# Kernel optimization log

Hardware: AMD Instinct MI355X
Metric: run time of the kernel (lower is better)

## Reference

```python
import jax, jax.numpy as jnp
import numpy as np

FEATS = 10
B, S, R = 64, 300, 100


def _linear_params(key, out_dim, in_dim):
    kw, kb = jax.random.split(key)
    bound = 1.0 / np.sqrt(in_dim)
    w = jax.random.uniform(kw, (out_dim, in_dim), jnp.float32, -bound, bound)
    b = jax.random.uniform(kb, (out_dim,), jnp.float32, -bound, bound)
    return w, b


def setup_inputs() -> dict:
    key = jax.random.key(0)
    ks = jax.random.split(key, 7)
    x = jax.random.normal(ks[0], (B, S, R, FEATS), jnp.float32)
    l1_w, l1_b = _linear_params(ks[1], 5, FEATS + 5)
    l2_w, l2_b = _linear_params(ks[2], 5, 5)
    l3_w, l3_b = _linear_params(ks[3], 5, 5)
    fc1_w, fc1_b = _linear_params(ks[4], 5, FEATS + 10)
    fc2_w, fc2_b = _linear_params(ks[5], 5, 5)
    fc3_w, fc3_b = _linear_params(ks[6], 1, 5)
    return {"x": x,
            "l1_w": l1_w, "l1_b": l1_b, "l2_w": l2_w, "l2_b": l2_b,
            "l3_w": l3_w, "l3_b": l3_b,
            "fc1_w": fc1_w, "fc1_b": fc1_b, "fc2_w": fc2_w, "fc2_b": fc2_b,
            "fc3_w": fc3_w, "fc3_b": fc3_b}


def reference(x, l1_w, l1_b, l2_w, l2_b, l3_w, l3_b,
              fc1_w, fc1_b, fc2_w, fc2_b, fc3_w, fc3_b):
    elu = jax.nn.elu
    bsz, seq, reads, _ = x.shape
    # dot of each read's first 4 feats with read 0's -> [B,S,R]
    r = jnp.sum(x[..., 0:4] * x[:, :, 0:1, 0:4], axis=-1)
    z = jnp.concatenate([r[..., None], x], axis=3)  # [B,S,R,feats+1]
    b = jnp.mean(x[..., 0:4], axis=2)               # [B,S,4]
    bexp = jnp.broadcast_to(b[:, :, None, :], (bsz, seq, reads, 4))
    bx = jnp.concatenate([bexp, z], axis=3)         # [B,S,R,feats+5]
    y = elu(jnp.einsum('bsrf,of->bsro', bx, l1_w) + l1_b)
    y = elu(jnp.einsum('bsrf,of->bsro', y, l2_w) + l2_b + y)
    y = elu(jnp.einsum('bsrf,of->bsro', y, l3_w) + l3_b + y)
    ymean = jnp.mean(y, axis=2, keepdims=True)      # [B,S,1,5]
    ymexp = jnp.broadcast_to(ymean, (bsz, seq, reads, 5))
    z2 = jnp.concatenate([ymexp, bx], axis=3)       # [B,S,R,feats+10]
    h = elu(jnp.einsum('bsrf,of->bsro', z2, fc1_w) + fc1_b)
    h = elu(jnp.einsum('bsrf,of->bsro', h, fc2_w) + fc2_b + h)
    h = 5.0 * elu(jnp.einsum('bsrf,of->bsro', h, fc3_w) + fc3_b)  # [B,S,R,1]
    out = jax.nn.sigmoid(jnp.max(h, axis=1))        # [B,R,1]
    return jnp.squeeze(out, axis=-1)                # [B,R]
```

## Files before the change

### kernel.cpp

```cpp
#include <hip/hip_runtime.h>
#include <math.h>

#define B 64
#define S 300
#define R 100
#define F 10
#define RF (R * F)
#define NTILE (B * S)
#define NWAVE (NTILE / 2)
#define NBLK (NWAVE / 4)

typedef float v2 __attribute__((ext_vector_type(2)));
typedef float v4 __attribute__((ext_vector_type(4)));

__device__ __forceinline__ v4 splat4(float s) { v4 r; r.x = s; r.y = s; r.z = s; r.w = s; return r; }
__device__ __forceinline__ v4 hsplat(float a, float b) { v4 r; r.x = a; r.y = a; r.z = b; r.w = b; return r; }
__device__ __forceinline__ v4 fma4(v4 a, float b, v4 c) {
    return __builtin_elementwise_fma(a, splat4(b), c);
}
__device__ __forceinline__ v4 fma4v(v4 a, v4 b, v4 c) {
    return __builtin_elementwise_fma(a, b, c);
}
__device__ __forceinline__ v4 elu4(v4 x) {
    v4 xm = __builtin_elementwise_min(x, splat4(0.f));
    v4 e;
    e.x = __expf(xm.x); e.y = __expf(xm.y); e.z = __expf(xm.z); e.w = __expf(xm.w);
    return __builtin_elementwise_max(x, e - splat4(1.f));
}

template <int CTRL>
__device__ __forceinline__ float dppadd(float v) {
    int t = __builtin_amdgcn_update_dpp(0, __float_as_int(v), CTRL, 0xF, 0xF, true);
    return v + __int_as_float(t);
}
__device__ __forceinline__ float wsum_dpp(float v) {
    v = dppadd<0x111>(v);
    v = dppadd<0x112>(v);
    v = dppadd<0x114>(v);
    v = dppadd<0x118>(v);
    v = dppadd<0x142>(v);
    v = dppadd<0x143>(v);
    return __uint_as_float(__builtin_amdgcn_readlane(__float_as_uint(v), 63));
}
__device__ __forceinline__ float rdlane0(float v) {
    return __uint_as_float(__builtin_amdgcn_readlane(__float_as_uint(v), 0));
}
__device__ __forceinline__ unsigned int fkey(float f) {
    unsigned int bits = __float_as_uint(f);
    return (bits & 0x80000000u) ? ~bits : (bits | 0x80000000u);
}

__global__ __launch_bounds__(256) void alt_pred_k1(
    const float* __restrict__ x,
    const float* __restrict__ l1_w, const float* __restrict__ l1_b,
    const float* __restrict__ l2_w, const float* __restrict__ l2_b,
    const float* __restrict__ l3_w, const float* __restrict__ l3_b,
    const float* __restrict__ fc1_w, const float* __restrict__ fc1_b,
    const float* __restrict__ fc2_w, const float* __restrict__ fc2_b,
    const float* __restrict__ fc3_w, const float* __restrict__ fc3_b,
    unsigned int* __restrict__ wsmax)
{
    const int tid = threadIdx.x;
    const int wv = tid >> 6;
    const int lane = tid & 63;
    const int gw = blockIdx.x * 4 + wv;
    const int t0 = gw * 2;
    const int b = t0 / S;
    const float* xA = x + (size_t)t0 * RF;
    const float* xB = xA + RF;

    const bool a2 = (lane < R - 64);
    const int r2 = a2 ? (lane + 64) : (R - 1);

    v4 f[F];
    {
        const float2* pA1 = (const float2*)(xA + lane * F);
        const float2* pA2 = (const float2*)(xA + r2 * F);
        const float2* pB1 = (const float2*)(xB + lane * F);
        const float2* pB2 = (const float2*)(xB + r2 * F);
#pragma unroll
        for (int i = 0; i < F; i += 2) {
            float2 a1 = pA1[i >> 1], a2v = pA2[i >> 1];
            float2 b1 = pB1[i >> 1], b2v = pB2[i >> 1];
            f[i].x = a1.x;     f[i].y = a2v.x; f[i].z = b1.x;     f[i].w = b2v.x;
            f[i + 1].x = a1.y; f[i + 1].y = a2v.y; f[i + 1].z = b1.y; f[i + 1].w = b2v.y;
        }
    }

    float x0A[4], x0B[4];
#pragma unroll
    for (int k = 0; k < 4; ++k) {
        x0A[k] = rdlane0(f[k].x);
        x0B[k] = rdlane0(f[k].z);
    }
    v4 rdot = f[3] * hsplat(x0A[3], x0B[3]);
    rdot = fma4v(f[2], hsplat(x0A[2], x0B[2]), rdot);
    rdot = fma4v(f[1], hsplat(x0A[1], x0B[1]), rdot);
    rdot = fma4v(f[0], hsplat(x0A[0], x0B[0]), rdot);

    float bmA[4], bmB[4];
#pragma unroll
    for (int k = 0; k < 4; ++k) {
        float locA = f[k].x + (a2 ? f[k].y : 0.f);
        float locB = f[k].z + (a2 ? f[k].w : 0.f);
        bmA[k] = wsum_dpp(locA) * (1.f / R);
        bmB[k] = wsum_dpp(locB) * (1.f / R);
    }

    v4 y1[5];
#pragma unroll
    for (int o = 0; o < 5; ++o) {
        float pA = l1_b[o], pB = l1_b[o];
#pragma unroll
        for (int k = 0; k < 4; ++k) {
            pA = fmaf(bmA[k], l1_w[o * 15 + k], pA);
            pB = fmaf(bmB[k], l1_w[o * 15 + k], pB);
        }
        v4 acc = hsplat(pA, pB);
        acc = fma4(rdot, l1_w[o * 15 + 4], acc);
#pragma unroll
        for (int k = 0; k < F; ++k) acc = fma4(f[k], l1_w[o * 15 + 5 + k], acc);
        y1[o] = elu4(acc);
    }
    v4 y2[5];
#pragma unroll
    for (int o = 0; o < 5; ++o) {
        v4 acc = splat4(l2_b[o]) + y1[o];
#pragma unroll
        for (int k = 0; k < 5; ++k) acc = fma4(y1[k], l2_w[o * 5 + k], acc);
        y2[o] = elu4(acc);
    }
    v4 y3[5];
#pragma unroll
    for (int o = 0; o < 5; ++o) {
        v4 acc = splat4(l3_b[o]) + y2[o];
#pragma unroll
        for (int k = 0; k < 5; ++k) acc = fma4(y2[k], l3_w[o * 5 + k], acc);
        y3[o] = elu4(acc);
    }

    float ymA[5], ymB[5];
#pragma unroll
    for (int k = 0; k < 5; ++k) {
        float locA = y3[k].x + (a2 ? y3[k].y : 0.f);
        float locB = y3[k].z + (a2 ? y3[k].w : 0.f);
        ymA[k] = wsum_dpp(locA) * (1.f / R);
        ymB[k] = wsum_dpp(locB) * (1.f / R);
    }

    v4 h1[5];
#pragma unroll
    for (int o = 0; o < 5; ++o) {
        float pA = fc1_b[o], pB = fc1_b[o];
#pragma unroll
        for (int k = 0; k < 5; ++k) {
            pA = fmaf(ymA[k], fc1_w[o * 20 + k], pA);
            pB = fmaf(ymB[k], fc1_w[o * 20 + k], pB);
        }
#pragma unroll
        for (int k = 0; k < 4; ++k) {
            pA = fmaf(bmA[k], fc1_w[o * 20 + 5 + k], pA);
            pB = fmaf(bmB[k], fc1_w[o * 20 + 5 + k], pB);
        }
        v4 acc = hsplat(pA, pB);
        acc = fma4(rdot, fc1_w[o * 20 + 9], acc);
#pragma unroll
        for (int k = 0; k < F; ++k) acc = fma4(f[k], fc1_w[o * 20 + 10 + k], acc);
        h1[o] = elu4(acc);
    }
    v4 h2[5];
#pragma unroll
    for (int o = 0; o < 5; ++o) {
        v4 acc = splat4(fc2_b[o]) + h1[o];
#pragma unroll
        for (int k = 0; k < 5; ++k) acc = fma4(h1[k], fc2_w[o * 5 + k], acc);
        h2[o] = elu4(acc);
    }
    v4 hacc = splat4(fc3_b[0]);
#pragma unroll
    for (int k = 0; k < 5; ++k) hacc = fma4(h2[k], fc3_w[k], hacc);

    const float m1 = fmaxf(hacc.x, hacc.z);
    const float m2 = fmaxf(hacc.y, hacc.w);
    atomicMax(&wsmax[b * R + lane], fkey(m1));
    if (a2) atomicMax(&wsmax[b * R + lane + 64], fkey(m2));
}

__global__ void alt_pred_k2(const unsigned int* __restrict__ wsmax,
                            float* __restrict__ out)
{
    const int i = blockIdx.x * blockDim.x + threadIdx.x;
    if (i < B * R) {
        const unsigned int key = wsmax[i];
        const unsigned int bits = (key & 0x80000000u) ? (key & 0x7FFFFFFFu) : ~key;
        const float acc = __uint_as_float(bits);
        const float h = 5.f * (acc > 0.f ? acc : (__expf(acc) - 1.f));
        out[i] = 1.f / (1.f + __expf(-h));
    }
}

extern "C" void kernel_launch(void* const* d_in, const int* in_sizes, int n_in,
                              void* d_out, int out_size, void* d_ws, size_t ws_size,
                              hipStream_t stream) {
    const float* x     = (const float*)d_in[0];
    const float* l1_w  = (const float*)d_in[1];
    const float* l1_b  = (const float*)d_in[2];
    const float* l2_w  = (const float*)d_in[3];
    const float* l2_b  = (const float*)d_in[4];
    const float* l3_w  = (const float*)d_in[5];
    const float* l3_b  = (const float*)d_in[6];
    const float* fc1_w = (const float*)d_in[7];
    const float* fc1_b = (const float*)d_in[8];
    const float* fc2_w = (const float*)d_in[9];
    const float* fc2_b = (const float*)d_in[10];
    const float* fc3_w = (const float*)d_in[11];
    const float* fc3_b = (const float*)d_in[12];

    unsigned int* wsmax = (unsigned int*)d_ws;
    hipMemsetAsync(d_ws, 0, (size_t)B * R * sizeof(unsigned int), stream);

    alt_pred_k1<<<NBLK, 256, 0, stream>>>(
        x, l1_w, l1_b, l2_w, l2_b, l3_w, l3_b,
        fc1_w, fc1_b, fc2_w, fc2_b, fc3_w, fc3_b, wsmax);

    alt_pred_k2<<<(B * R + 255) / 256, 256, 0, stream>>>(wsmax, (float*)d_out);
}
```

Measured before the change: 41.37 us.

## Repack per-lane data as float2 pairs, shrink blocks, load read0 directly

Reorganizes per-lane state from 4-wide vectors into lo/hi float2 pairs grouped by tile (A,B), so packed FMA ops pair the two tiles. Block size drops from 256 to 128 threads with twice as many blocks. Read 0's features are loaded straight from memory with a uniform base instead of readlane, the partial-mean mask is applied with an FMA, and ELU uses exp2f with a log2e prescale. It aims to improve packed-math use, scheduling and occupancy, but adds an extra global load per tile and changes block granularity.

```diff
diff --git a/kernel.cpp b/kernel.cpp
--- a/kernel.cpp
+++ b/kernel.cpp
@@ -8,49 +8,49 @@
 #define RF (R * F)
 #define NTILE (B * S)
 #define NWAVE (NTILE / 2)
-#define NBLK (NWAVE / 4)
-
-typedef float v2 __attribute__((ext_vector_type(2)));
-typedef float v4 __attribute__((ext_vector_type(4)));
-
-__device__ __forceinline__ v4 splat4(float s) { v4 r; r.x = s; r.y = s; r.z = s; r.w = s; return r; }
-__device__ __forceinline__ v4 hsplat(float a, float b) { v4 r; r.x = a; r.y = a; r.z = b; r.w = b; return r; }
-__device__ __forceinline__ v4 fma4(v4 a, float b, v4 c) {
-    return __builtin_elementwise_fma(a, splat4(b), c);
-}
-__device__ __forceinline__ v4 fma4v(v4 a, v4 b, v4 c) {
+#define NBLK (NWAVE / 2)
+
+typedef float v2f __attribute__((ext_vector_type(2)));
+
+#define LOG2E 1.44269504088896340736f
+
+__device__ __forceinline__ v2f splat2(float s) { v2f r; r.x = s; r.y = s; return r; }
+__device__ __forceinline__ v2f fma2s(v2f a, float b, v2f c) {
+    return __builtin_elementwise_fma(a, splat2(b), c);
+}
+__device__ __forceinline__ v2f fma2v(v2f a, v2f b, v2f c) {
     return __builtin_elementwise_fma(a, b, c);
 }
-__device__ __forceinline__ v4 elu4(v4 x) {
-    v4 xm = __builtin_elementwise_min(x, splat4(0.f));
-    v4 e;
-    e.x = __expf(xm.x); e.y = __expf(xm.y); e.z = __expf(xm.z); e.w = __expf(xm.w);
-    return __builtin_elementwise_max(x, e - splat4(1.f));
+__device__ __forceinline__ v2f elu2(v2f x) {
+    v2f t = __builtin_elementwise_min(x, splat2(0.f)) * splat2(LOG2E);
+    v2f e; e.x = exp2f(t.x); e.y = exp2f(t.y);
+    return __builtin_elementwise_max(x, e - splat2(1.f));
 }
 
 template <int CTRL>
-__device__ __forceinline__ float dppadd(float v) {
-    int t = __builtin_amdgcn_update_dpp(0, __float_as_int(v), CTRL, 0xF, 0xF, true);
-    return v + __int_as_float(t);
-}
-__device__ __forceinline__ float wsum_dpp(float v) {
-    v = dppadd<0x111>(v);
-    v = dppadd<0x112>(v);
-    v = dppadd<0x114>(v);
-    v = dppadd<0x118>(v);
-    v = dppadd<0x142>(v);
-    v = dppadd<0x143>(v);
-    return __uint_as_float(__builtin_amdgcn_readlane(__float_as_uint(v), 63));
-}
-__device__ __forceinline__ float rdlane0(float v) {
-    return __uint_as_float(__builtin_amdgcn_readlane(__float_as_uint(v), 0));
+__device__ __forceinline__ v2f dppadd2(v2f v) {
+    int tx = __builtin_amdgcn_update_dpp(0, __float_as_int(v.x), CTRL, 0xF, 0xF, true);
+    int ty = __builtin_amdgcn_update_dpp(0, __float_as_int(v.y), CTRL, 0xF, 0xF, true);
+    v2f t; t.x = __int_as_float(tx); t.y = __int_as_float(ty);
+    return v + t;
+}
+__device__ __forceinline__ void wmean2(v2f v, float& a, float& b) {
+    v = dppadd2<0x111>(v);
+    v = dppadd2<0x112>(v);
+    v = dppadd2<0x114>(v);
+    v = dppadd2<0x118>(v);
+    v = dppadd2<0x142>(v);
+    v = dppadd2<0x143>(v);
+    v = v * splat2(1.f / R);
+    a = __uint_as_float(__builtin_amdgcn_readlane(__float_as_uint(v.x), 63));
+    b = __uint_as_float(__builtin_amdgcn_readlane(__float_as_uint(v.y), 63));
 }
 __device__ __forceinline__ unsigned int fkey(float f) {
     unsigned int bits = __float_as_uint(f);
     return (bits & 0x80000000u) ? ~bits : (bits | 0x80000000u);
 }
 
-__global__ __launch_bounds__(256) void alt_pred_k1(
+__global__ __launch_bounds__(128) void alt_pred_k1(
     const float* __restrict__ x,
     const float* __restrict__ l1_w, const float* __restrict__ l1_b,
     const float* __restrict__ l2_w, const float* __restrict__ l2_b,
@@ -61,53 +61,55 @@
     unsigned int* __restrict__ wsmax)
 {
     const int tid = threadIdx.x;
-    const int wv = tid >> 6;
     const int lane = tid & 63;
-    const int gw = blockIdx.x * 4 + wv;
-    const int t0 = gw * 2;
+    const int t0 = __builtin_amdgcn_readfirstlane((blockIdx.x * 2 + (tid >> 6)) * 2);
     const int b = t0 / S;
     const float* xA = x + (size_t)t0 * RF;
     const float* xB = xA + RF;
 
     const bool a2 = (lane < R - 64);
     const int r2 = a2 ? (lane + 64) : (R - 1);
-
-    v4 f[F];
+    const v2f msk2 = splat2(a2 ? 1.f : 0.f);
+
+    float x0A[4], x0B[4];
+#pragma unroll
+    for (int k = 0; k < 4; ++k) { x0A[k] = xA[k]; x0B[k] = xB[k]; }
+
+    v2f f_lo[F], f_hi[F];
     {
         const float2* pA1 = (const float2*)(xA + lane * F);
         const float2* pA2 = (const float2*)(xA + r2 * F);
         const float2* pB1 = (const float2*)(xB + lane * F);
         const float2* pB2 = (const float2*)(xB + r2 * F);
 #pragma unroll
-        for (int i = 0; i < F; i += 2) {
-            float2 a1 = pA1[i >> 1], a2v = pA2[i >> 1];
-            float2 b1 = pB1[i >> 1], b2v = pB2[i >> 1];
-            f[i].x = a1.x;     f[i].y = a2v.x; f[i].z = b1.x;     f[i].w = b2v.x;
-            f[i + 1].x = a1.y; f[i + 1].y = a2v.y; f[i + 1].z = b1.y; f[i + 1].w = b2v.y;
-        }
-    }
-
-    float x0A[4], x0B[4];
+        for (int i = 0; i < 5; ++i) {
+            float2 a1 = pA1[i], b1 = pB1[i], a2v = pA2[i], b2v = pB2[i];
+            f_lo[2 * i].x = a1.x;     f_lo[2 * i].y = b1.x;
+            f_lo[2 * i + 1].x = a1.y; f_lo[2 * i + 1].y = b1.y;
+            f_hi[2 * i].x = a2v.x;    f_hi[2 * i].y = b2v.x;
+            f_hi[2 * i + 1].x = a2v.y; f_hi[2 * i + 1].y = b2v.y;
+        }
+    }
+
+    v2f x0v[4];
+#pragma unroll
+    for (int k = 0; k < 4; ++k) { x0v[k].x = x0A[k]; x0v[k].y = x0B[k]; }
+    v2f rdot_lo = f_lo[3] * x0v[3];
+    v2f rdot_hi = f_hi[3] * x0v[3];
+#pragma unroll
+    for (int k = 2; k >= 0; --k) {
+        rdot_lo = fma2v(f_lo[k], x0v[k], rdot_lo);
+        rdot_hi = fma2v(f_hi[k], x0v[k], rdot_hi);
+    }
+
+    float bmA[4], bmB[4];
 #pragma unroll
     for (int k = 0; k < 4; ++k) {
-        x0A[k] = rdlane0(f[k].x);
-        x0B[k] = rdlane0(f[k].z);
-    }
-    v4 rdot = f[3] * hsplat(x0A[3], x0B[3]);
-    rdot = fma4v(f[2], hsplat(x0A[2], x0B[2]), rdot);
-    rdot = fma4v(f[1], hsplat(x0A[1], x0B[1]), rdot);
-    rdot = fma4v(f[0], hsplat(x0A[0], x0B[0]), rdot);
-
-    float bmA[4], bmB[4];
-#pragma unroll
-    for (int k = 0; k < 4; ++k) {
-        float locA = f[k].x + (a2 ? f[k].y : 0.f);
-        float locB = f[k].z + (a2 ? f[k].w : 0.f);
-        bmA[k] = wsum_dpp(locA) * (1.f / R);
-        bmB[k] = wsum_dpp(locB) * (1.f / R);
-    }
-
-    v4 y1[5];
+        v2f loc = fma2v(f_hi[k], msk2, f_lo[k]);
+        wmean2(loc, bmA[k], bmB[k]);
+    }
+
+    v2f y1_lo[5], y1_hi[5];
 #pragma unroll
     for (int o = 0; o < 5; ++o) {
         float pA = l1_b[o], pB = l1_b[o];
@@ -116,39 +118,49 @@
             pA = fmaf(bmA[k], l1_w[o * 15 + k], pA);
             pB = fmaf(bmB[k], l1_w[o * 15 + k], pB);
         }
-        v4 acc = hsplat(pA, pB);
-        acc = fma4(rdot, l1_w[o * 15 + 4], acc);
-#pragma unroll
-        for (int k = 0; k < F; ++k) acc = fma4(f[k], l1_w[o * 15 + 5 + k], acc);
-        y1[o] = elu4(acc);
-    }
-    v4 y2[5];
-#pragma unroll
-    for (int o = 0; o < 5; ++o) {
-        v4 acc = splat4(l2_b[o]) + y1[o];
-#pragma unroll
-        for (int k = 0; k < 5; ++k) acc = fma4(y1[k], l2_w[o * 5 + k], acc);
-        y2[o] = elu4(acc);
-    }
-    v4 y3[5];
-#pragma unroll
-    for (int o = 0; o < 5; ++o) {
-        v4 acc = splat4(l3_b[o]) + y2[o];
-#pragma unroll
-        for (int k = 0; k < 5; ++k) acc = fma4(y2[k], l3_w[o * 5 + k], acc);
-        y3[o] = elu4(acc);
+        v2f pre; pre.x = pA; pre.y = pB;
+        v2f alo = fma2s(rdot_lo, l1_w[o * 15 + 4], pre);
+        v2f ahi = fma2s(rdot_hi, l1_w[o * 15 + 4], pre);
+#pragma unroll
+        for (int k = 0; k < F; ++k) {
+            alo = fma2s(f_lo[k], l1_w[o * 15 + 5 + k], alo);
+            ahi = fma2s(f_hi[k], l1_w[o * 15 + 5 + k], ahi);
+        }
+        y1_lo[o] = elu2(alo); y1_hi[o] = elu2(ahi);
+    }
+    v2f y2_lo[5], y2_hi[5];
+#pragma unroll
+    for (int o = 0; o < 5; ++o) {
+        v2f alo = y1_lo[o] + splat2(l2_b[o]);
+        v2f ahi = y1_hi[o] + splat2(l2_b[o]);
+#pragma unroll
+        for (int k = 0; k < 5; ++k) {
+            alo = fma2s(y1_lo[k], l2_w[o * 5 + k], alo);
+            ahi = fma2s(y1_hi[k], l2_w[o * 5 + k], ahi);
+        }
+        y2_lo[o] = elu2(alo); y2_hi[o] = elu2(ahi);
+    }
+    v2f y3_lo[5], y3_hi[5];
+#pragma unroll
+    for (int o = 0; o < 5; ++o) {
+        v2f alo = y2_lo[o] + splat2(l3_b[o]);
+        v2f ahi = y2_hi[o] + splat2(l3_b[o]);
+#pragma unroll
+        for (int k = 0; k < 5; ++k) {
+            alo = fma2s(y2_lo[k], l3_w[o * 5 + k], alo);
+            ahi = fma2s(y2_hi[k], l3_w[o * 5 + k], ahi);
+        }
+        y3_lo[o] = elu2(alo); y3_hi[o] = elu2(ahi);
     }
 
     float ymA[5], ymB[5];
 #pragma unroll
     for (int k = 0; k < 5; ++k) {
-        float locA = y3[k].x + (a2 ? y3[k].y : 0.f);
-        float locB = y3[k].z + (a2 ? y3[k].w : 0.f);
-        ymA[k] = wsum_dpp(locA) * (1.f / R);
-        ymB[k] = wsum_dpp(locB) * (1.f / R);
-    }
-
-    v4 h1[5];
+        v2f loc = fma2v(y3_hi[k], msk2, y3_lo[k]);
+        wmean2(loc, ymA[k], ymB[k]);
+    }
+
+    v2f h1_lo[5], h1_hi[5];
 #pragma unroll
     for (int o = 0; o < 5; ++o) {
         float pA = fc1_b[o], pB = fc1_b[o];
@@ -162,26 +174,38 @@
             pA = fmaf(bmA[k], fc1_w[o * 20 + 5 + k], pA);
             pB = fmaf(bmB[k], fc1_w[o * 20 + 5 + k], pB);
         }
-        v4 acc = hsplat(pA, pB);
-        acc = fma4(rdot, fc1_w[o * 20 + 9], acc);
-#pragma unroll
-        for (int k = 0; k < F; ++k) acc = fma4(f[k], fc1_w[o * 20 + 10 + k], acc);
-        h1[o] = elu4(acc);
-    }
-    v4 h2[5];
-#pragma unroll
-    for (int o = 0; o < 5; ++o) {
-        v4 acc = splat4(fc2_b[o]) + h1[o];
-#pragma unroll
-        for (int k = 0; k < 5; ++k) acc = fma4(h1[k], fc2_w[o * 5 + k], acc);
-        h2[o] = elu4(acc);
-    }
-    v4 hacc = splat4(fc3_b[0]);
-#pragma unroll
-    for (int k = 0; k < 5; ++k) hacc = fma4(h2[k], fc3_w[k], hacc);
-
-    const float m1 = fmaxf(hacc.x, hacc.z);
-    const float m2 = fmaxf(hacc.y, hacc.w);
+        v2f pre; pre.x = pA; pre.y = pB;
+        v2f alo = fma2s(rdot_lo, fc1_w[o * 20 + 9], pre);
+        v2f ahi = fma2s(rdot_hi, fc1_w[o * 20 + 9], pre);
+#pragma unroll
+        for (int k = 0; k < F; ++k) {
+            alo = fma2s(f_lo[k], fc1_w[o * 20 + 10 + k], alo);
+            ahi = fma2s(f_hi[k], fc1_w[o * 20 + 10 + k], ahi);
+        }
+        h1_lo[o] = elu2(alo); h1_hi[o] = elu2(ahi);
+    }
+    v2f h2_lo[5], h2_hi[5];
+#pragma unroll
+    for (int o = 0; o < 5; ++o) {
+        v2f alo = h1_lo[o] + splat2(fc2_b[o]);
+        v2f ahi = h1_hi[o] + splat2(fc2_b[o]);
+#pragma unroll
+        for (int k = 0; k < 5; ++k) {
+            alo = fma2s(h1_lo[k], fc2_w[o * 5 + k], alo);
+            ahi = fma2s(h1_hi[k], fc2_w[o * 5 + k], ahi);
+        }
+        h2_lo[o] = elu2(alo); h2_hi[o] = elu2(ahi);
+    }
+    v2f hacc_lo = splat2(fc3_b[0]);
+    v2f hacc_hi = splat2(fc3_b[0]);
+#pragma unroll
+    for (int k = 0; k < 5; ++k) {
+        hacc_lo = fma2s(h2_lo[k], fc3_w[k], hacc_lo);
+        hacc_hi = fma2s(h2_hi[k], fc3_w[k], hacc_hi);
+    }
+
+    const float m1 = fmaxf(hacc_lo.x, hacc_lo.y);
+    const float m2 = fmaxf(hacc_hi.x, hacc_hi.y);
     atomicMax(&wsmax[b * R + lane], fkey(m1));
     if (a2) atomicMax(&wsmax[b * R + lane + 64], fkey(m2));
 }
@@ -219,7 +243,7 @@
     unsigned int* wsmax = (unsigned int*)d_ws;
     hipMemsetAsync(d_ws, 0, (size_t)B * R * sizeof(unsigned int), stream);
 
-    alt_pred_k1<<<NBLK, 256, 0, stream>>>(
+    alt_pred_k1<<<NBLK, 128, 0, stream>>>(
         x, l1_w, l1_b, l2_w, l2_b, l3_w, l3_b,
         fc1_w, fc1_b, fc2_w, fc2_b, fc3_w, fc3_b, wsmax);
 
```

New measurement: 48.50 us. +17.2%, slower.
